# Kernel tuning notes

Measured on AMD Instinct MI355X. Metric: run time of the kernel, lower is better.

The kernel has to match this reference:

```python
import jax, jax.numpy as jnp
import numpy as np

N = 100000      # nodes
E = 3200000     # edges (avg degree 32)
F_IN = 16       # node_feature_size
R1, R2, R3 = 8, 16, 8   # gcn hidden sizes
N1 = 32                  # mlp hidden


def _lin(k, fan_in, shape):
    s = 1.0 / np.sqrt(fan_in)
    return jax.random.uniform(k, shape, minval=-s, maxval=s, dtype=jnp.float32)


def setup_inputs() -> dict:
    key = jax.random.key(0)
    ks = jax.random.split(key, 16)
    x = jax.random.normal(ks[0], (N, F_IN), dtype=jnp.float32)
    edge_index = jax.random.randint(ks[1], (2, E), 0, N, dtype=jnp.int64)
    return {
        "x": x,
        "edge_index": edge_index,
        # GraphConv k: out = mean_agg(x_j) @ W_rel + b + x @ W_root  (PyG GraphConv, lin_root bias=False)
        "W_rel1": _lin(ks[2], F_IN, (F_IN, R1)), "b1": _lin(ks[3], F_IN, (R1,)), "W_root1": _lin(ks[4], F_IN, (F_IN, R1)),
        "W_rel2": _lin(ks[5], R1, (R1, R2)),   "b2": _lin(ks[6], R1, (R2,)),   "W_root2": _lin(ks[7], R1, (R1, R2)),
        "W_rel3": _lin(ks[8], R2, (R2, R3)),   "b3": _lin(ks[9], R2, (R3,)),   "W_root3": _lin(ks[10], R2, (R2, R3)),
        "fc1_W": _lin(ks[11], R3, (R3, N1)), "fc1_b": _lin(ks[12], R3, (N1,)),
        "fc2_W": _lin(ks[13], N1, (N1, 1)),  "fc2_b": _lin(ks[14], N1, (1,)),
    }


def _graph_conv(x, src, dst, W_rel, b, W_root):
    # message: gather source features; aggregate: mean over incoming edges at dst
    n = x.shape[0]
    msg_sum = jax.ops.segment_sum(x[src], dst, num_segments=n)          # [N, F]
    cnt = jax.ops.segment_sum(jnp.ones(src.shape, x.dtype), dst, num_segments=n)
    mean = msg_sum / jnp.maximum(cnt, 1.0)[:, None]
    return mean @ W_rel + b + x @ W_root


def reference(x, edge_index, W_rel1, b1, W_root1, W_rel2, b2, W_root2,
              W_rel3, b3, W_root3, fc1_W, fc1_b, fc2_W, fc2_b):
    src, dst = edge_index[0], edge_index[1]
    h = jax.nn.sigmoid(_graph_conv(x, src, dst, W_rel1, b1, W_root1))
    h = jax.nn.sigmoid(_graph_conv(h, src, dst, W_rel2, b2, W_root2))
    h = jax.nn.sigmoid(_graph_conv(h, src, dst, W_rel3, b3, W_root3))
    h = jax.nn.sigmoid(h @ fc1_W + fc1_b)
    return h @ fc2_W + fc2_b   # [N, 1]
```

## Files before the change

### kernel.cpp

```cpp
#include <hip/hip_runtime.h>
#include <math.h>


#define CHUNK     16384
#define BW        128
#define MAXNB     800
#define MAXB_RAW  5376
#define MAXB_PAD  5760
#define REGION    5760

typedef _Float16 half8 __attribute__((ext_vector_type(8)));

static __device__ __forceinline__ float sigmoidf_(float x) {
    return 1.0f / (1.0f + expf(-x));
}

static __device__ __forceinline__ int scan256_excl(int v, int* s) {
    int tid = threadIdx.x;
    s[tid] = v;
    for (int off = 1; off < 256; off <<= 1) {
        __syncthreads();
        int t = (tid >= off) ? s[tid - off] : 0;
        __syncthreads();
        s[tid] += t;
    }
    __syncthreads();
    return s[tid] - v;
}

static __device__ __forceinline__ void gather_sum8(
    const half8* __restrict__ t, const int* __restrict__ csr,
    int rs, int from, int to, float* s) {
#pragma unroll
    for (int c = 0; c < 8; ++c) s[c] = 0.0f;
    int e = from;
    for (; e + 4 <= to; e += 4) {
        int4 ci = *(const int4*)(csr + rs + e);
        half8 v0 = t[ci.x]; half8 v1 = t[ci.y];
        half8 v2 = t[ci.z]; half8 v3 = t[ci.w];
#pragma unroll
        for (int c = 0; c < 8; ++c)
            s[c] += ((float)v0[c] + (float)v1[c]) + ((float)v2[c] + (float)v3[c]);
    }
    for (; e < to; ++e) {
        half8 v = t[csr[rs + e]];
#pragma unroll
        for (int c = 0; c < 8; ++c) s[c] += (float)v[c];
    }
}

static __device__ __forceinline__ void quad_gather_mean8(
    const half8* __restrict__ t, const int* __restrict__ csr,
    int rs, int d, int q, float* s) {
    int qs = ((d + 15) >> 4) << 2;
    int from = q * qs; if (from > d) from = d;
    int to = from + qs; if (to > d) to = d;
    gather_sum8(t, csr, rs, from, to, s);
#pragma unroll
    for (int c = 0; c < 8; ++c) s[c] += __shfl_xor(s[c], 1);
#pragma unroll
    for (int c = 0; c < 8; ++c) s[c] += __shfl_xor(s[c], 2);
    float inv = 1.0f / (float)(d > 0 ? d : 1);
#pragma unroll
    for (int c = 0; c < 8; ++c) s[c] *= inv;
}

__global__ __launch_bounds__(512)
void setup_scatter_kernel(const float* __restrict__ x, const float* __restrict__ Wrel,
                          const float* __restrict__ bias, const float* __restrict__ Wroot,
                          _Float16* __restrict__ t1, _Float16* __restrict__ z1,
                          const int* __restrict__ src, const int* __restrict__ dst,
                          int* __restrict__ gcur, unsigned* __restrict__ stage,
                          int N, int E, int NB, int nbT) {
    __shared__ float sWr[128], sWo[128], sb[8];
    __shared__ int s_hist[MAXNB];
    __shared__ int s_cur[MAXNB];
    int tid = threadIdx.x, blk = blockIdx.x;

    if (blk < nbT) {
        if (tid < 128) { sWr[tid] = Wrel[tid]; sWo[tid] = Wroot[tid]; }
        if (tid >= 128 && tid < 136) sb[tid - 128] = bias[tid - 128];
        __syncthreads();
        int node = blk * 512 + tid;
        if (node >= N) return;
        const float4* x4 = (const float4*)x;
        float xv[16];
#pragma unroll
        for (int k = 0; k < 4; ++k) {
            float4 v = x4[node * 4 + k];
            xv[4 * k] = v.x; xv[4 * k + 1] = v.y; xv[4 * k + 2] = v.z; xv[4 * k + 3] = v.w;
        }
        float ta[8], za[8];
#pragma unroll
        for (int j = 0; j < 8; ++j) { ta[j] = 0.0f; za[j] = sb[j]; }
#pragma unroll
        for (int f = 0; f < 16; ++f) {
            float xf = xv[f];
#pragma unroll
            for (int j = 0; j < 8; ++j) {
                ta[j] += xf * sWr[f * 8 + j];
                za[j] += xf * sWo[f * 8 + j];
            }
        }
        half8 th, zh;
#pragma unroll
        for (int j = 0; j < 8; ++j) { th[j] = (_Float16)ta[j]; zh[j] = (_Float16)za[j]; }
        ((half8*)t1)[node] = th;
        ((half8*)z1)[node] = zh;
    } else {
        int chunk = blk - nbT;
        int base = chunk * CHUNK;
        int cnt = E - base; if (cnt > CHUNK) cnt = CHUNK;
        for (int i = tid; i < NB; i += 512) s_hist[i] = 0;
        __syncthreads();
        if (cnt == CHUNK) {
            const int4* d4 = (const int4*)(dst + base);
#pragma unroll
            for (int k = 0; k < CHUNK / 2048; ++k) {
                int4 d = d4[k * 512 + tid];
                atomicAdd(&s_hist[d.x >> 7], 1);
                atomicAdd(&s_hist[d.y >> 7], 1);
                atomicAdd(&s_hist[d.z >> 7], 1);
                atomicAdd(&s_hist[d.w >> 7], 1);
            }
        } else {
            for (int i = tid; i < cnt; i += 512) atomicAdd(&s_hist[dst[base + i] >> 7], 1);
        }
        __syncthreads();
        for (int i = tid; i < NB; i += 512) {
            int hh = s_hist[i];
            s_cur[i] = i * REGION + atomicAdd(&gcur[i], hh);
        }
        __syncthreads();
        if (cnt == CHUNK) {
            const int4* d4 = (const int4*)(dst + base);
            const int4* s4 = (const int4*)(src + base);
#pragma unroll
            for (int k = 0; k < CHUNK / 2048; ++k) {
                int4 d = d4[k * 512 + tid];
                int4 s = s4[k * 512 + tid];
                int dd[4] = {d.x, d.y, d.z, d.w};
                int ss[4] = {s.x, s.y, s.z, s.w};
#pragma unroll
                for (int j = 0; j < 4; ++j) {
                    int pos = atomicAdd(&s_cur[dd[j] >> 7], 1);
                    stage[pos] = ((unsigned)(dd[j] & 127) << 17) | (unsigned)ss[j];
                }
            }
        } else {
            for (int i = tid; i < cnt; i += 512) {
                int d = dst[base + i], s = src[base + i];
                int pos = atomicAdd(&s_cur[d >> 7], 1);
                stage[pos] = ((unsigned)(d & 127) << 17) | (unsigned)s;
            }
        }
    }
}

__global__ __launch_bounds__(256)
void csr_agg1_kernel(const unsigned* __restrict__ stage, const int* __restrict__ gcur,
                     int* __restrict__ csr, int* __restrict__ deg,
                     int* __restrict__ rowstart,
                     const _Float16* __restrict__ t1, const _Float16* __restrict__ z1,
                     _Float16* __restrict__ h1, int N) {
    __shared__ unsigned __attribute__((aligned(16))) s_p[MAXB_RAW];
    __shared__ int __attribute__((aligned(16))) s_out[MAXB_PAD];
    __shared__ int h[BW], hs[BW], curb[BW];
    __shared__ int s_scan[256];
    int b = blockIdx.x, tid = threadIdx.x;
    int beg = b * REGION;
    int tot = gcur[b]; if (tot > MAXB_RAW) tot = MAXB_RAW;

    const uint4* st4 = (const uint4*)(stage + beg);
    int n4 = tot >> 2;
    for (int i = tid; i < n4; i += 256) ((uint4*)s_p)[i] = st4[i];
    for (int i = (n4 << 2) + tid; i < tot; i += 256) s_p[i] = stage[beg + i];
    if (tid < BW) h[tid] = 0;
    __syncthreads();

    for (int i = tid; i < tot; i += 256) atomicAdd(&h[s_p[i] >> 17], 1);
    __syncthreads();

    int v = (tid < BW) ? ((h[tid] + 3) & ~3) : 0;
    int excl = scan256_excl(v, s_scan);
    int ptot = s_scan[255];
    int dg = 0, myStart = 0;
    if (tid < BW) {
        dg = h[tid]; myStart = excl;
        hs[tid] = myStart; curb[tid] = myStart;
        int node = b * BW + tid;
        if (node < N) { deg[node] = dg; rowstart[node] = beg + myStart; }
    }
    __syncthreads();

    for (int i = tid; i < tot; i += 256) {
        unsigned p = s_p[i];
        int pos = atomicAdd(&curb[p >> 17], 1);
        s_out[pos] = (int)(p & 0x1FFFF);
    }
    __syncthreads();

    if (ptot > MAXB_PAD) ptot = MAXB_PAD;
    int p4 = ptot >> 2;
    int4* csr4 = (int4*)(csr + beg);
    for (int i = tid; i < p4; i += 256) csr4[i] = ((const int4*)s_out)[i];

    int nd = tid >> 1, half = tid & 1;
    int node = b * BW + nd;
    if (node < N) {
        int rs = hs[nd], d = h[nd];
        int d1 = ((d >> 1) + 3) & ~3; if (d1 > d) d1 = d;
        int from = half ? d1 : 0;
        int to   = half ? d  : d1;
        const half8* t = (const half8*)t1;
        float s[8];
#pragma unroll
        for (int c = 0; c < 8; ++c) s[c] = 0.0f;
        int e = from;
        for (; e + 4 <= to; e += 4) {
            int4 ci = *(const int4*)(s_out + rs + e);
            half8 v0 = t[ci.x]; half8 v1 = t[ci.y];
            half8 v2 = t[ci.z]; half8 v3 = t[ci.w];
#pragma unroll
            for (int c = 0; c < 8; ++c)
                s[c] += ((float)v0[c] + (float)v1[c]) + ((float)v2[c] + (float)v3[c]);
        }
        for (; e < to; ++e) {
            half8 vv = t[s_out[rs + e]];
#pragma unroll
            for (int c = 0; c < 8; ++c) s[c] += (float)vv[c];
        }
#pragma unroll
        for (int c = 0; c < 8; ++c) s[c] += __shfl_xor(s[c], 1);
        if (half == 0) {
            float inv = 1.0f / (float)(d > 0 ? d : 1);
            half8 z = ((const half8*)z1)[node];
            half8 o;
#pragma unroll
            for (int c = 0; c < 8; ++c) o[c] = (_Float16)sigmoidf_(s[c] * inv + (float)z[c]);
            ((half8*)h1)[node] = o;
        }
    }
}

__global__ __launch_bounds__(256)
void gcn2_fused_kernel(const _Float16* __restrict__ h1,
                       const int* __restrict__ rowstart, const int* __restrict__ deg,
                       const int* __restrict__ csr,
                       const float* __restrict__ W2r, const float* __restrict__ b2,
                       const float* __restrict__ W2o,
                       const float* __restrict__ W3r, const float* __restrict__ b3,
                       const float* __restrict__ W3o,
                       _Float16* __restrict__ t3, _Float16* __restrict__ z3, int n) {
    __shared__ float sW2r[128], sW2o[128], sW3r[128], sW3o[128], sb2[16], sb3[8];
    int tid = threadIdx.x;
    if (tid < 128) {
        sW2r[tid] = W2r[tid]; sW2o[tid] = W2o[tid];
        sW3r[tid] = W3r[tid]; sW3o[tid] = W3o[tid];
    }
    if (tid < 16) sb2[tid] = b2[tid];
    if (tid < 8) sb3[tid] = b3[tid];
    __syncthreads();
    int idx = blockIdx.x * 256 + tid;
    int node = idx >> 2, q = idx & 3;
    if (node >= n) return;

    float m[8];
    quad_gather_mean8((const half8*)h1, csr, rowstart[node], deg[node], q, m);
    half8 sf = ((const half8*)h1)[node];
    float x8[8];
#pragma unroll
    for (int c = 0; c < 8; ++c) x8[c] = (float)sf[c];

    float v16[16];
#pragma unroll
    for (int j = 0; j < 16; ++j) {
        float a = sb2[j];
#pragma unroll
        for (int f = 0; f < 8; ++f)
            a += m[f] * sW2r[f * 16 + j] + x8[f] * sW2o[f * 16 + j];
        v16[j] = sigmoidf_(a);
    }
    float ta[8], za[8];
#pragma unroll
    for (int j = 0; j < 8; ++j) { ta[j] = 0.0f; za[j] = sb3[j]; }
#pragma unroll
    for (int f = 0; f < 16; ++f) {
        float hv = v16[f];
#pragma unroll
        for (int j = 0; j < 8; ++j) {
            ta[j] += hv * sW3r[f * 8 + j];
            za[j] += hv * sW3o[f * 8 + j];
        }
    }
    if (q) return;
    half8 th, zh;
#pragma unroll
    for (int j = 0; j < 8; ++j) { th[j] = (_Float16)ta[j]; zh[j] = (_Float16)za[j]; }
    ((half8*)t3)[node] = th;
    ((half8*)z3)[node] = zh;
}

__global__ __launch_bounds__(256)
void agg3_mlp_kernel(const _Float16* __restrict__ t3, const _Float16* __restrict__ z3,
                     const int* __restrict__ rowstart, const int* __restrict__ deg,
                     const int* __restrict__ csr,
                     const float* __restrict__ fc1W, const float* __restrict__ fc1b,
                     const float* __restrict__ fc2W, const float* __restrict__ fc2b,
                     float* __restrict__ out, int n) {
    __shared__ float sW1[256], sb1[32], sW2[32];
    __shared__ float sb2_;
    int tid = threadIdx.x;
    if (tid < 256) sW1[tid] = fc1W[tid];
    if (tid < 32) { sb1[tid] = fc1b[tid]; sW2[tid] = fc2W[tid]; }
    if (tid == 0) sb2_ = fc2b[0];
    __syncthreads();
    int idx = blockIdx.x * 256 + tid;
    int node = idx >> 2, q = idx & 3;
    if (node >= n) return;

    float s[8];
    quad_gather_mean8((const half8*)t3, csr, rowstart[node], deg[node], q, s);
    half8 z = ((const half8*)z3)[node];
    float h[8];
#pragma unroll
    for (int c = 0; c < 8; ++c) h[c] = sigmoidf_(s[c] + (float)z[c]);

    float acc = sb2_;
#pragma unroll
    for (int j = 0; j < 32; ++j) {
        float a = sb1[j];
#pragma unroll
        for (int f = 0; f < 8; ++f) a += h[f] * sW1[f * 32 + j];
        acc += sW2[j] * sigmoidf_(a);
    }
    if (q == 0) out[node] = acc;
}

extern "C" void kernel_launch(void* const* d_in, const int* in_sizes, int n_in,
                              void* d_out, int out_size, void* d_ws, size_t ws_size,
                              hipStream_t stream) {
    const float* x      = (const float*)d_in[0];
    const int*   ei     = (const int*)d_in[1];
    const float* Wrel1  = (const float*)d_in[2];
    const float* b1     = (const float*)d_in[3];
    const float* Wroot1 = (const float*)d_in[4];
    const float* Wrel2  = (const float*)d_in[5];
    const float* b2     = (const float*)d_in[6];
    const float* Wroot2 = (const float*)d_in[7];
    const float* Wrel3  = (const float*)d_in[8];
    const float* b3     = (const float*)d_in[9];
    const float* Wroot3 = (const float*)d_in[10];
    const float* fc1W   = (const float*)d_in[11];
    const float* fc1b   = (const float*)d_in[12];
    const float* fc2W   = (const float*)d_in[13];
    const float* fc2b   = (const float*)d_in[14];
    float* out = (float*)d_out;

    const int N = in_sizes[0] / 16;
    const int E = in_sizes[1] / 2;
    const int* e_src = ei;
    const int* e_dst = ei + E;

    const int NB   = (N + BW - 1) / BW;
    const int NBLK = (E + CHUNK - 1) / CHUNK;
    const int nbT  = (N + 511) / 512;
    const int nbQ  = (4 * N + 255) / 256;

    char* ws = (char*)d_ws;
    size_t off = 0;
    auto alloc = [&](size_t bytes) { char* p = ws + off; off += (bytes + 15) & ~size_t(15); return p; };
    unsigned* stage = (unsigned*)alloc((size_t)NB * REGION * 4);
    int* csr        = (int*)alloc((size_t)NB * REGION * 4);
    int* gcur       = (int*)alloc((size_t)NB * 4);
    int* deg        = (int*)alloc((size_t)N * 4);
    int* rowstart   = (int*)alloc((size_t)N * 4);
    _Float16* t1    = (_Float16*)alloc((size_t)N * 8 * 2);
    _Float16* z1    = (_Float16*)alloc((size_t)N * 8 * 2);
    _Float16* h1    = (_Float16*)alloc((size_t)N * 8 * 2);
    _Float16* t3    = (_Float16*)alloc((size_t)N * 8 * 2);
    _Float16* z3    = (_Float16*)alloc((size_t)N * 8 * 2);

    hipMemsetAsync(gcur, 0, (size_t)NB * 4, stream);

    setup_scatter_kernel<<<nbT + NBLK, 512, 0, stream>>>(
        x, Wrel1, b1, Wroot1, t1, z1, e_src, e_dst, gcur, stage, N, E, NB, nbT);
    csr_agg1_kernel<<<NB, 256, 0, stream>>>(stage, gcur, csr, deg, rowstart,
                                            t1, z1, h1, N);
    gcn2_fused_kernel<<<nbQ, 256, 0, stream>>>(h1, rowstart, deg, csr,
                                               Wrel2, b2, Wroot2, Wrel3, b3, Wroot3, t3, z3, N);
    agg3_mlp_kernel<<<nbQ, 256, 0, stream>>>(t3, z3, rowstart, deg, csr,
                                             fc1W, fc1b, fc2W, fc2b, out, N);
}
```

Before: 223.5 us.

## Fuse CSR build and three aggregation layers into one persistent kernel with grid barriers

Merges the CSR-build/layer-1 kernel, the layer-2/3 kernel and the final aggregation+MLP kernel into a single kernel. Grid-wide atomic barriers separate the layers, and each block keeps its bucket's CSR in shared memory so it is never written to or re-read from global memory. Buckets grow to 256 nodes with 512-thread blocks, so NB blocks are about 391, and all of them must be co-resident for the spin barrier to avoid deadlock. The raw staged pairs are no longer copied into LDS; they are read twice from global memory instead. The change removes two launches and the global CSR traffic, at the cost of the barrier waits and a deadlock risk if the blocks are not all resident.

```diff
diff --git a/kernel.cpp b/kernel.cpp
--- a/kernel.cpp
+++ b/kernel.cpp
@@ -2,12 +2,12 @@
 #include <math.h>
 
 
-#define CHUNK     16384
-#define BW        128
-#define MAXNB     800
-#define MAXB_RAW  5376
-#define MAXB_PAD  5760
-#define REGION    5760
+#define CHUNK    32768
+#define BW       256
+#define NBMAX    400
+#define MAXB_RAW 9216
+#define MAXB_PAD 9984
+#define REGION   9472
 
 typedef _Float16 half8 __attribute__((ext_vector_type(8)));
 
@@ -15,54 +15,15 @@
     return 1.0f / (1.0f + expf(-x));
 }
 
-static __device__ __forceinline__ int scan256_excl(int v, int* s) {
-    int tid = threadIdx.x;
-    s[tid] = v;
-    for (int off = 1; off < 256; off <<= 1) {
-        __syncthreads();
-        int t = (tid >= off) ? s[tid - off] : 0;
-        __syncthreads();
-        s[tid] += t;
-    }
-    __syncthreads();
-    return s[tid] - v;
-}
-
-static __device__ __forceinline__ void gather_sum8(
-    const half8* __restrict__ t, const int* __restrict__ csr,
-    int rs, int from, int to, float* s) {
-#pragma unroll
-    for (int c = 0; c < 8; ++c) s[c] = 0.0f;
-    int e = from;
-    for (; e + 4 <= to; e += 4) {
-        int4 ci = *(const int4*)(csr + rs + e);
-        half8 v0 = t[ci.x]; half8 v1 = t[ci.y];
-        half8 v2 = t[ci.z]; half8 v3 = t[ci.w];
-#pragma unroll
-        for (int c = 0; c < 8; ++c)
-            s[c] += ((float)v0[c] + (float)v1[c]) + ((float)v2[c] + (float)v3[c]);
-    }
-    for (; e < to; ++e) {
-        half8 v = t[csr[rs + e]];
-#pragma unroll
-        for (int c = 0; c < 8; ++c) s[c] += (float)v[c];
-    }
-}
-
-static __device__ __forceinline__ void quad_gather_mean8(
-    const half8* __restrict__ t, const int* __restrict__ csr,
-    int rs, int d, int q, float* s) {
-    int qs = ((d + 15) >> 4) << 2;
-    int from = q * qs; if (from > d) from = d;
-    int to = from + qs; if (to > d) to = d;
-    gather_sum8(t, csr, rs, from, to, s);
-#pragma unroll
-    for (int c = 0; c < 8; ++c) s[c] += __shfl_xor(s[c], 1);
-#pragma unroll
-    for (int c = 0; c < 8; ++c) s[c] += __shfl_xor(s[c], 2);
-    float inv = 1.0f / (float)(d > 0 ? d : 1);
-#pragma unroll
-    for (int c = 0; c < 8; ++c) s[c] *= inv;
+static __device__ __forceinline__ void gbar(int* bar, int target) {
+    __syncthreads();
+    if (threadIdx.x == 0) {
+        __threadfence();
+        __hip_atomic_fetch_add(bar, 1, __ATOMIC_ACQ_REL, __HIP_MEMORY_SCOPE_AGENT);
+        while (__hip_atomic_load(bar, __ATOMIC_ACQUIRE, __HIP_MEMORY_SCOPE_AGENT) < target)
+            __builtin_amdgcn_s_sleep(32);
+    }
+    __syncthreads();
 }
 
 __global__ __launch_bounds__(512)
@@ -73,8 +34,8 @@
                           int* __restrict__ gcur, unsigned* __restrict__ stage,
                           int N, int E, int NB, int nbT) {
     __shared__ float sWr[128], sWo[128], sb[8];
-    __shared__ int s_hist[MAXNB];
-    __shared__ int s_cur[MAXNB];
+    __shared__ int s_hist[NBMAX];
+    __shared__ int s_cur[NBMAX];
     int tid = threadIdx.x, blk = blockIdx.x;
 
     if (blk < nbT) {
@@ -118,13 +79,13 @@
 #pragma unroll
             for (int k = 0; k < CHUNK / 2048; ++k) {
                 int4 d = d4[k * 512 + tid];
-                atomicAdd(&s_hist[d.x >> 7], 1);
-                atomicAdd(&s_hist[d.y >> 7], 1);
-                atomicAdd(&s_hist[d.z >> 7], 1);
-                atomicAdd(&s_hist[d.w >> 7], 1);
+                atomicAdd(&s_hist[d.x >> 8], 1);
+                atomicAdd(&s_hist[d.y >> 8], 1);
+                atomicAdd(&s_hist[d.z >> 8], 1);
+                atomicAdd(&s_hist[d.w >> 8], 1);
             }
         } else {
-            for (int i = tid; i < cnt; i += 512) atomicAdd(&s_hist[dst[base + i] >> 7], 1);
+            for (int i = tid; i < cnt; i += 512) atomicAdd(&s_hist[dst[base + i] >> 8], 1);
         }
         __syncthreads();
         for (int i = tid; i < NB; i += 512) {
@@ -143,75 +104,102 @@
                 int ss[4] = {s.x, s.y, s.z, s.w};
 #pragma unroll
                 for (int j = 0; j < 4; ++j) {
-                    int pos = atomicAdd(&s_cur[dd[j] >> 7], 1);
-                    stage[pos] = ((unsigned)(dd[j] & 127) << 17) | (unsigned)ss[j];
+                    int pos = atomicAdd(&s_cur[dd[j] >> 8], 1);
+                    stage[pos] = ((unsigned)(dd[j] & 255) << 17) | (unsigned)ss[j];
                 }
             }
         } else {
             for (int i = tid; i < cnt; i += 512) {
                 int d = dst[base + i], s = src[base + i];
-                int pos = atomicAdd(&s_cur[d >> 7], 1);
-                stage[pos] = ((unsigned)(d & 127) << 17) | (unsigned)s;
-            }
-        }
-    }
-}
-
-__global__ __launch_bounds__(256)
-void csr_agg1_kernel(const unsigned* __restrict__ stage, const int* __restrict__ gcur,
-                     int* __restrict__ csr, int* __restrict__ deg,
-                     int* __restrict__ rowstart,
-                     const _Float16* __restrict__ t1, const _Float16* __restrict__ z1,
-                     _Float16* __restrict__ h1, int N) {
-    __shared__ unsigned __attribute__((aligned(16))) s_p[MAXB_RAW];
+                int pos = atomicAdd(&s_cur[d >> 8], 1);
+                stage[pos] = ((unsigned)(d & 255) << 17) | (unsigned)s;
+            }
+        }
+    }
+}
+
+__global__ __launch_bounds__(512, 4)
+void mega_kernel(const unsigned* __restrict__ stage, const int* __restrict__ gcur,
+                 int* __restrict__ bar,
+                 const _Float16* __restrict__ t1, const _Float16* __restrict__ z1,
+                 _Float16* __restrict__ h1, _Float16* __restrict__ t3,
+                 _Float16* __restrict__ z3,
+                 const float* __restrict__ W2r, const float* __restrict__ b2,
+                 const float* __restrict__ W2o,
+                 const float* __restrict__ W3r, const float* __restrict__ b3,
+                 const float* __restrict__ W3o,
+                 const float* __restrict__ fc1W, const float* __restrict__ fc1b,
+                 const float* __restrict__ fc2W, const float* __restrict__ fc2b,
+                 float* __restrict__ out, int N, int NB) {
     __shared__ int __attribute__((aligned(16))) s_out[MAXB_PAD];
     __shared__ int h[BW], hs[BW], curb[BW];
-    __shared__ int s_scan[256];
+    __shared__ int s_scan[512];
+    __shared__ float sW2r[128], sW2o[128], sW3r[128], sW3o[128], sb2[16], sb3[8];
+    __shared__ float sW1[256], sb1[32], sW2m[32], sb2s[1];
+
     int b = blockIdx.x, tid = threadIdx.x;
     int beg = b * REGION;
     int tot = gcur[b]; if (tot > MAXB_RAW) tot = MAXB_RAW;
 
+    if (tid < 128) { sW2r[tid] = W2r[tid]; sW2o[tid] = W2o[tid];
+                     sW3r[tid] = W3r[tid]; sW3o[tid] = W3o[tid]; }
+    if (tid < 256) sW1[tid] = fc1W[tid];
+    if (tid < 32) { sb1[tid] = fc1b[tid]; sW2m[tid] = fc2W[tid]; }
+    if (tid < 16) sb2[tid] = b2[tid];
+    if (tid < 8)  sb3[tid] = b3[tid];
+    if (tid == 0) sb2s[0] = fc2b[0];
+    if (tid < BW) h[tid] = 0;
+    __syncthreads();
+
     const uint4* st4 = (const uint4*)(stage + beg);
     int n4 = tot >> 2;
-    for (int i = tid; i < n4; i += 256) ((uint4*)s_p)[i] = st4[i];
-    for (int i = (n4 << 2) + tid; i < tot; i += 256) s_p[i] = stage[beg + i];
-    if (tid < BW) h[tid] = 0;
-    __syncthreads();
-
-    for (int i = tid; i < tot; i += 256) atomicAdd(&h[s_p[i] >> 17], 1);
+    for (int i = tid; i < n4; i += 512) {
+        uint4 p = st4[i];
+        atomicAdd(&h[p.x >> 17], 1); atomicAdd(&h[p.y >> 17], 1);
+        atomicAdd(&h[p.z >> 17], 1); atomicAdd(&h[p.w >> 17], 1);
+    }
+    for (int i = (n4 << 2) + tid; i < tot; i += 512) atomicAdd(&h[stage[beg + i] >> 17], 1);
     __syncthreads();
 
     int v = (tid < BW) ? ((h[tid] + 3) & ~3) : 0;
-    int excl = scan256_excl(v, s_scan);
-    int ptot = s_scan[255];
-    int dg = 0, myStart = 0;
-    if (tid < BW) {
-        dg = h[tid]; myStart = excl;
-        hs[tid] = myStart; curb[tid] = myStart;
-        int node = b * BW + tid;
-        if (node < N) { deg[node] = dg; rowstart[node] = beg + myStart; }
-    }
-    __syncthreads();
-
-    for (int i = tid; i < tot; i += 256) {
-        unsigned p = s_p[i];
+    s_scan[tid] = v;
+    for (int off = 1; off < 512; off <<= 1) {
+        __syncthreads();
+        int t = (tid >= off) ? s_scan[tid - off] : 0;
+        __syncthreads();
+        s_scan[tid] += t;
+    }
+    __syncthreads();
+    if (tid < BW) { int myS = s_scan[tid] - v; hs[tid] = myS; curb[tid] = myS; }
+    __syncthreads();
+
+    for (int i = tid; i < n4; i += 512) {
+        uint4 p = st4[i];
+        int pos;
+        pos = atomicAdd(&curb[p.x >> 17], 1); s_out[pos] = (int)(p.x & 0x1FFFF);
+        pos = atomicAdd(&curb[p.y >> 17], 1); s_out[pos] = (int)(p.y & 0x1FFFF);
+        pos = atomicAdd(&curb[p.z >> 17], 1); s_out[pos] = (int)(p.z & 0x1FFFF);
+        pos = atomicAdd(&curb[p.w >> 17], 1); s_out[pos] = (int)(p.w & 0x1FFFF);
+    }
+    for (int i = (n4 << 2) + tid; i < tot; i += 512) {
+        unsigned p = stage[beg + i];
         int pos = atomicAdd(&curb[p >> 17], 1);
         s_out[pos] = (int)(p & 0x1FFFF);
     }
     __syncthreads();
 
-    if (ptot > MAXB_PAD) ptot = MAXB_PAD;
-    int p4 = ptot >> 2;
-    int4* csr4 = (int4*)(csr + beg);
-    for (int i = tid; i < p4; i += 256) csr4[i] = ((const int4*)s_out)[i];
-
     int nd = tid >> 1, half = tid & 1;
     int node = b * BW + nd;
+    int rs = 0, d = 0, from = 0, to = 0;
     if (node < N) {
-        int rs = hs[nd], d = h[nd];
+        rs = hs[nd]; d = h[nd];
         int d1 = ((d >> 1) + 3) & ~3; if (d1 > d) d1 = d;
-        int from = half ? d1 : 0;
-        int to   = half ? d  : d1;
+        from = half ? d1 : 0;
+        to   = half ? d  : d1;
+    }
+    float inv = 1.0f / (float)(d > 0 ? d : 1);
+
+    if (node < N) {
         const half8* t = (const half8*)t1;
         float s[8];
 #pragma unroll
@@ -219,8 +207,7 @@
         int e = from;
         for (; e + 4 <= to; e += 4) {
             int4 ci = *(const int4*)(s_out + rs + e);
-            half8 v0 = t[ci.x]; half8 v1 = t[ci.y];
-            half8 v2 = t[ci.z]; half8 v3 = t[ci.w];
+            half8 v0 = t[ci.x], v1 = t[ci.y], v2 = t[ci.z], v3 = t[ci.w];
 #pragma unroll
             for (int c = 0; c < 8; ++c)
                 s[c] += ((float)v0[c] + (float)v1[c]) + ((float)v2[c] + (float)v3[c]);
@@ -233,7 +220,6 @@
 #pragma unroll
         for (int c = 0; c < 8; ++c) s[c] += __shfl_xor(s[c], 1);
         if (half == 0) {
-            float inv = 1.0f / (float)(d > 0 ? d : 1);
             half8 z = ((const half8*)z1)[node];
             half8 o;
 #pragma unroll
@@ -241,100 +227,100 @@
             ((half8*)h1)[node] = o;
         }
     }
-}
-
-__global__ __launch_bounds__(256)
-void gcn2_fused_kernel(const _Float16* __restrict__ h1,
-                       const int* __restrict__ rowstart, const int* __restrict__ deg,
-                       const int* __restrict__ csr,
-                       const float* __restrict__ W2r, const float* __restrict__ b2,
-                       const float* __restrict__ W2o,
-                       const float* __restrict__ W3r, const float* __restrict__ b3,
-                       const float* __restrict__ W3o,
-                       _Float16* __restrict__ t3, _Float16* __restrict__ z3, int n) {
-    __shared__ float sW2r[128], sW2o[128], sW3r[128], sW3o[128], sb2[16], sb3[8];
-    int tid = threadIdx.x;
-    if (tid < 128) {
-        sW2r[tid] = W2r[tid]; sW2o[tid] = W2o[tid];
-        sW3r[tid] = W3r[tid]; sW3o[tid] = W3o[tid];
-    }
-    if (tid < 16) sb2[tid] = b2[tid];
-    if (tid < 8) sb3[tid] = b3[tid];
-    __syncthreads();
-    int idx = blockIdx.x * 256 + tid;
-    int node = idx >> 2, q = idx & 3;
-    if (node >= n) return;
-
-    float m[8];
-    quad_gather_mean8((const half8*)h1, csr, rowstart[node], deg[node], q, m);
-    half8 sf = ((const half8*)h1)[node];
-    float x8[8];
-#pragma unroll
-    for (int c = 0; c < 8; ++c) x8[c] = (float)sf[c];
-
-    float v16[16];
-#pragma unroll
-    for (int j = 0; j < 16; ++j) {
-        float a = sb2[j];
-#pragma unroll
-        for (int f = 0; f < 8; ++f)
-            a += m[f] * sW2r[f * 16 + j] + x8[f] * sW2o[f * 16 + j];
-        v16[j] = sigmoidf_(a);
-    }
-    float ta[8], za[8];
-#pragma unroll
-    for (int j = 0; j < 8; ++j) { ta[j] = 0.0f; za[j] = sb3[j]; }
-#pragma unroll
-    for (int f = 0; f < 16; ++f) {
-        float hv = v16[f];
-#pragma unroll
-        for (int j = 0; j < 8; ++j) {
-            ta[j] += hv * sW3r[f * 8 + j];
-            za[j] += hv * sW3o[f * 8 + j];
-        }
-    }
-    if (q) return;
-    half8 th, zh;
-#pragma unroll
-    for (int j = 0; j < 8; ++j) { th[j] = (_Float16)ta[j]; zh[j] = (_Float16)za[j]; }
-    ((half8*)t3)[node] = th;
-    ((half8*)z3)[node] = zh;
-}
-
-__global__ __launch_bounds__(256)
-void agg3_mlp_kernel(const _Float16* __restrict__ t3, const _Float16* __restrict__ z3,
-                     const int* __restrict__ rowstart, const int* __restrict__ deg,
-                     const int* __restrict__ csr,
-                     const float* __restrict__ fc1W, const float* __restrict__ fc1b,
-                     const float* __restrict__ fc2W, const float* __restrict__ fc2b,
-                     float* __restrict__ out, int n) {
-    __shared__ float sW1[256], sb1[32], sW2[32];
-    __shared__ float sb2_;
-    int tid = threadIdx.x;
-    if (tid < 256) sW1[tid] = fc1W[tid];
-    if (tid < 32) { sb1[tid] = fc1b[tid]; sW2[tid] = fc2W[tid]; }
-    if (tid == 0) sb2_ = fc2b[0];
-    __syncthreads();
-    int idx = blockIdx.x * 256 + tid;
-    int node = idx >> 2, q = idx & 3;
-    if (node >= n) return;
-
-    float s[8];
-    quad_gather_mean8((const half8*)t3, csr, rowstart[node], deg[node], q, s);
-    half8 z = ((const half8*)z3)[node];
-    float h[8];
-#pragma unroll
-    for (int c = 0; c < 8; ++c) h[c] = sigmoidf_(s[c] + (float)z[c]);
-
-    float acc = sb2_;
-#pragma unroll
-    for (int j = 0; j < 32; ++j) {
-        float a = sb1[j];
-#pragma unroll
-        for (int f = 0; f < 8; ++f) a += h[f] * sW1[f * 32 + j];
-        acc += sW2[j] * sigmoidf_(a);
-    }
-    if (q == 0) out[node] = acc;
+    gbar(bar, NB);
+
+    if (node < N) {
+        const half8* t = (const half8*)h1;
+        float s[8];
+#pragma unroll
+        for (int c = 0; c < 8; ++c) s[c] = 0.0f;
+        int e = from;
+        for (; e + 4 <= to; e += 4) {
+            int4 ci = *(const int4*)(s_out + rs + e);
+            half8 v0 = t[ci.x], v1 = t[ci.y], v2 = t[ci.z], v3 = t[ci.w];
+#pragma unroll
+            for (int c = 0; c < 8; ++c)
+                s[c] += ((float)v0[c] + (float)v1[c]) + ((float)v2[c] + (float)v3[c]);
+        }
+        for (; e < to; ++e) {
+            half8 vv = t[s_out[rs + e]];
+#pragma unroll
+            for (int c = 0; c < 8; ++c) s[c] += (float)vv[c];
+        }
+#pragma unroll
+        for (int c = 0; c < 8; ++c) s[c] += __shfl_xor(s[c], 1);
+        float m[8];
+#pragma unroll
+        for (int c = 0; c < 8; ++c) m[c] = s[c] * inv;
+        half8 sf = ((const half8*)h1)[node];
+        float x8[8];
+#pragma unroll
+        for (int c = 0; c < 8; ++c) x8[c] = (float)sf[c];
+        float v16[16];
+#pragma unroll
+        for (int j = 0; j < 16; ++j) {
+            float a = sb2[j];
+#pragma unroll
+            for (int f = 0; f < 8; ++f)
+                a += m[f] * sW2r[f * 16 + j] + x8[f] * sW2o[f * 16 + j];
+            v16[j] = sigmoidf_(a);
+        }
+        float ta[8], za[8];
+#pragma unroll
+        for (int j = 0; j < 8; ++j) { ta[j] = 0.0f; za[j] = sb3[j]; }
+#pragma unroll
+        for (int f = 0; f < 16; ++f) {
+            float hv = v16[f];
+#pragma unroll
+            for (int j = 0; j < 8; ++j) {
+                ta[j] += hv * sW3r[f * 8 + j];
+                za[j] += hv * sW3o[f * 8 + j];
+            }
+        }
+        if (half == 0) {
+            half8 th, zh;
+#pragma unroll
+            for (int j = 0; j < 8; ++j) { th[j] = (_Float16)ta[j]; zh[j] = (_Float16)za[j]; }
+            ((half8*)t3)[node] = th;
+            ((half8*)z3)[node] = zh;
+        }
+    }
+    gbar(bar, 2 * NB);
+
+    if (node < N) {
+        const half8* t = (const half8*)t3;
+        float s[8];
+#pragma unroll
+        for (int c = 0; c < 8; ++c) s[c] = 0.0f;
+        int e = from;
+        for (; e + 4 <= to; e += 4) {
+            int4 ci = *(const int4*)(s_out + rs + e);
+            half8 v0 = t[ci.x], v1 = t[ci.y], v2 = t[ci.z], v3 = t[ci.w];
+#pragma unroll
+            for (int c = 0; c < 8; ++c)
+                s[c] += ((float)v0[c] + (float)v1[c]) + ((float)v2[c] + (float)v3[c]);
+        }
+        for (; e < to; ++e) {
+            half8 vv = t[s_out[rs + e]];
+#pragma unroll
+            for (int c = 0; c < 8; ++c) s[c] += (float)vv[c];
+        }
+#pragma unroll
+        for (int c = 0; c < 8; ++c) s[c] += __shfl_xor(s[c], 1);
+        half8 z = ((const half8*)z3)[node];
+        float hv8[8];
+#pragma unroll
+        for (int c = 0; c < 8; ++c) hv8[c] = sigmoidf_(s[c] * inv + (float)z[c]);
+        float acc = sb2s[0];
+#pragma unroll
+        for (int j = 0; j < 32; ++j) {
+            float a = sb1[j];
+#pragma unroll
+            for (int f = 0; f < 8; ++f) a += hv8[f] * sW1[f * 32 + j];
+            acc += sW2m[j] * sigmoidf_(a);
+        }
+        if (half == 0) out[node] = acc;
+    }
 }
 
 extern "C" void kernel_launch(void* const* d_in, const int* in_sizes, int n_in,
@@ -365,30 +351,26 @@
     const int NB   = (N + BW - 1) / BW;
     const int NBLK = (E + CHUNK - 1) / CHUNK;
     const int nbT  = (N + 511) / 512;
-    const int nbQ  = (4 * N + 255) / 256;
 
     char* ws = (char*)d_ws;
     size_t off = 0;
     auto alloc = [&](size_t bytes) { char* p = ws + off; off += (bytes + 15) & ~size_t(15); return p; };
     unsigned* stage = (unsigned*)alloc((size_t)NB * REGION * 4);
-    int* csr        = (int*)alloc((size_t)NB * REGION * 4);
-    int* gcur       = (int*)alloc((size_t)NB * 4);
-    int* deg        = (int*)alloc((size_t)N * 4);
-    int* rowstart   = (int*)alloc((size_t)N * 4);
+    int* gcur       = (int*)alloc(((size_t)NB + 8) * 4);
+    int* bar        = gcur + NB;
     _Float16* t1    = (_Float16*)alloc((size_t)N * 8 * 2);
     _Float16* z1    = (_Float16*)alloc((size_t)N * 8 * 2);
     _Float16* h1    = (_Float16*)alloc((size_t)N * 8 * 2);
     _Float16* t3    = (_Float16*)alloc((size_t)N * 8 * 2);
     _Float16* z3    = (_Float16*)alloc((size_t)N * 8 * 2);
 
-    hipMemsetAsync(gcur, 0, (size_t)NB * 4, stream);
+    hipMemsetAsync(gcur, 0, ((size_t)NB + 8) * 4, stream);
 
     setup_scatter_kernel<<<nbT + NBLK, 512, 0, stream>>>(
         x, Wrel1, b1, Wroot1, t1, z1, e_src, e_dst, gcur, stage, N, E, NB, nbT);
-    csr_agg1_kernel<<<NB, 256, 0, stream>>>(stage, gcur, csr, deg, rowstart,
-                                            t1, z1, h1, N);
-    gcn2_fused_kernel<<<nbQ, 256, 0, stream>>>(h1, rowstart, deg, csr,
-                                               Wrel2, b2, Wroot2, Wrel3, b3, Wroot3, t3, z3, N);
-    agg3_mlp_kernel<<<nbQ, 256, 0, stream>>>(t3, z3, rowstart, deg, csr,
-                                             fc1W, fc1b, fc2W, fc2b, out, N);
-}
+
+    mega_kernel<<<NB, 512, 0, stream>>>(
+        stage, gcur, bar, t1, z1, h1, t3, z3,
+        Wrel2, b2, Wroot2, Wrel3, b3, Wroot3,
+        fc1W, fc1b, fc2W, fc2b, out, N, NB);
+}
```

Measured after the change: 337.3 us. +50.9%, slower.

## Widen per-node gather parallelism and double scatter chunk size

Applied to the files above, without the earlier changes.

Doubles the edge chunk size in the scatter stage. The CSR/aggregation-1 kernel moves to 512 threads, using four lanes per node instead of two. Layer-2 and final aggregation kernels use eight lanes per node instead of four, and non-leader lanes return early after the reduction so the dense tail math runs once per node. The aim is more memory-level parallelism in the latency-bound gathers and less redundant per-lane compute, at the cost of an extra shuffle stage, a longer block scan and fewer scatter blocks.

```diff
diff --git a/kernel.cpp b/kernel.cpp
--- a/kernel.cpp
+++ b/kernel.cpp
@@ -2,7 +2,7 @@
 #include <math.h>
 
 
-#define CHUNK     16384
+#define CHUNK     32768
 #define BW        128
 #define MAXNB     800
 #define MAXB_RAW  5376
@@ -13,19 +13,6 @@
 
 static __device__ __forceinline__ float sigmoidf_(float x) {
     return 1.0f / (1.0f + expf(-x));
-}
-
-static __device__ __forceinline__ int scan256_excl(int v, int* s) {
-    int tid = threadIdx.x;
-    s[tid] = v;
-    for (int off = 1; off < 256; off <<= 1) {
-        __syncthreads();
-        int t = (tid >= off) ? s[tid - off] : 0;
-        __syncthreads();
-        s[tid] += t;
-    }
-    __syncthreads();
-    return s[tid] - v;
 }
 
 static __device__ __forceinline__ void gather_sum8(
@@ -49,17 +36,19 @@
     }
 }
 
-static __device__ __forceinline__ void quad_gather_mean8(
+static __device__ __forceinline__ void oct_gather_mean8(
     const half8* __restrict__ t, const int* __restrict__ csr,
-    int rs, int d, int q, float* s) {
-    int qs = ((d + 15) >> 4) << 2;
-    int from = q * qs; if (from > d) from = d;
+    int rs, int d, int oc, float* s) {
+    int qs = ((d + 31) >> 5) << 2;
+    int from = oc * qs; if (from > d) from = d;
     int to = from + qs; if (to > d) to = d;
     gather_sum8(t, csr, rs, from, to, s);
 #pragma unroll
     for (int c = 0; c < 8; ++c) s[c] += __shfl_xor(s[c], 1);
 #pragma unroll
     for (int c = 0; c < 8; ++c) s[c] += __shfl_xor(s[c], 2);
+#pragma unroll
+    for (int c = 0; c < 8; ++c) s[c] += __shfl_xor(s[c], 4);
     float inv = 1.0f / (float)(d > 0 ? d : 1);
 #pragma unroll
     for (int c = 0; c < 8; ++c) s[c] *= inv;
@@ -157,7 +146,7 @@
     }
 }
 
-__global__ __launch_bounds__(256)
+__global__ __launch_bounds__(512)
 void csr_agg1_kernel(const unsigned* __restrict__ stage, const int* __restrict__ gcur,
                      int* __restrict__ csr, int* __restrict__ deg,
                      int* __restrict__ rowstart,
@@ -166,34 +155,40 @@
     __shared__ unsigned __attribute__((aligned(16))) s_p[MAXB_RAW];
     __shared__ int __attribute__((aligned(16))) s_out[MAXB_PAD];
     __shared__ int h[BW], hs[BW], curb[BW];
-    __shared__ int s_scan[256];
+    __shared__ int s_scan[512];
     int b = blockIdx.x, tid = threadIdx.x;
     int beg = b * REGION;
     int tot = gcur[b]; if (tot > MAXB_RAW) tot = MAXB_RAW;
 
     const uint4* st4 = (const uint4*)(stage + beg);
     int n4 = tot >> 2;
-    for (int i = tid; i < n4; i += 256) ((uint4*)s_p)[i] = st4[i];
-    for (int i = (n4 << 2) + tid; i < tot; i += 256) s_p[i] = stage[beg + i];
+    for (int i = tid; i < n4; i += 512) ((uint4*)s_p)[i] = st4[i];
+    for (int i = (n4 << 2) + tid; i < tot; i += 512) s_p[i] = stage[beg + i];
     if (tid < BW) h[tid] = 0;
     __syncthreads();
 
-    for (int i = tid; i < tot; i += 256) atomicAdd(&h[s_p[i] >> 17], 1);
+    for (int i = tid; i < tot; i += 512) atomicAdd(&h[s_p[i] >> 17], 1);
     __syncthreads();
 
     int v = (tid < BW) ? ((h[tid] + 3) & ~3) : 0;
-    int excl = scan256_excl(v, s_scan);
-    int ptot = s_scan[255];
-    int dg = 0, myStart = 0;
+    s_scan[tid] = v;
+    for (int off = 1; off < 512; off <<= 1) {
+        __syncthreads();
+        int t = (tid >= off) ? s_scan[tid - off] : 0;
+        __syncthreads();
+        s_scan[tid] += t;
+    }
+    __syncthreads();
+    int ptot = s_scan[511];
     if (tid < BW) {
-        dg = h[tid]; myStart = excl;
-        hs[tid] = myStart; curb[tid] = myStart;
+        int myS = s_scan[tid] - v;
+        hs[tid] = myS; curb[tid] = myS;
         int node = b * BW + tid;
-        if (node < N) { deg[node] = dg; rowstart[node] = beg + myStart; }
-    }
-    __syncthreads();
-
-    for (int i = tid; i < tot; i += 256) {
+        if (node < N) { deg[node] = h[tid]; rowstart[node] = beg + myS; }
+    }
+    __syncthreads();
+
+    for (int i = tid; i < tot; i += 512) {
         unsigned p = s_p[i];
         int pos = atomicAdd(&curb[p >> 17], 1);
         s_out[pos] = (int)(p & 0x1FFFF);
@@ -203,15 +198,15 @@
     if (ptot > MAXB_PAD) ptot = MAXB_PAD;
     int p4 = ptot >> 2;
     int4* csr4 = (int4*)(csr + beg);
-    for (int i = tid; i < p4; i += 256) csr4[i] = ((const int4*)s_out)[i];
-
-    int nd = tid >> 1, half = tid & 1;
+    for (int i = tid; i < p4; i += 512) csr4[i] = ((const int4*)s_out)[i];
+
+    int nd = tid >> 2, q = tid & 3;
     int node = b * BW + nd;
     if (node < N) {
         int rs = hs[nd], d = h[nd];
-        int d1 = ((d >> 1) + 3) & ~3; if (d1 > d) d1 = d;
-        int from = half ? d1 : 0;
-        int to   = half ? d  : d1;
+        int qs = ((d + 15) >> 4) << 2;
+        int from = q * qs; if (from > d) from = d;
+        int to = from + qs; if (to > d) to = d;
         const half8* t = (const half8*)t1;
         float s[8];
 #pragma unroll
@@ -232,7 +227,9 @@
         }
 #pragma unroll
         for (int c = 0; c < 8; ++c) s[c] += __shfl_xor(s[c], 1);
-        if (half == 0) {
+#pragma unroll
+        for (int c = 0; c < 8; ++c) s[c] += __shfl_xor(s[c], 2);
+        if (q == 0) {
             float inv = 1.0f / (float)(d > 0 ? d : 1);
             half8 z = ((const half8*)z1)[node];
             half8 o;
@@ -262,11 +259,11 @@
     if (tid < 8) sb3[tid] = b3[tid];
     __syncthreads();
     int idx = blockIdx.x * 256 + tid;
-    int node = idx >> 2, q = idx & 3;
+    int node = idx >> 3, oc = idx & 7;
     if (node >= n) return;
 
     float m[8];
-    quad_gather_mean8((const half8*)h1, csr, rowstart[node], deg[node], q, m);
+    oct_gather_mean8((const half8*)h1, csr, rowstart[node], deg[node], oc, m);
     half8 sf = ((const half8*)h1)[node];
     float x8[8];
 #pragma unroll
@@ -281,6 +278,7 @@
             a += m[f] * sW2r[f * 16 + j] + x8[f] * sW2o[f * 16 + j];
         v16[j] = sigmoidf_(a);
     }
+    if (oc) return;
     float ta[8], za[8];
 #pragma unroll
     for (int j = 0; j < 8; ++j) { ta[j] = 0.0f; za[j] = sb3[j]; }
@@ -293,7 +291,6 @@
             za[j] += hv * sW3o[f * 8 + j];
         }
     }
-    if (q) return;
     half8 th, zh;
 #pragma unroll
     for (int j = 0; j < 8; ++j) { th[j] = (_Float16)ta[j]; zh[j] = (_Float16)za[j]; }
@@ -316,11 +313,12 @@
     if (tid == 0) sb2_ = fc2b[0];
     __syncthreads();
     int idx = blockIdx.x * 256 + tid;
-    int node = idx >> 2, q = idx & 3;
+    int node = idx >> 3, oc = idx & 7;
     if (node >= n) return;
 
     float s[8];
-    quad_gather_mean8((const half8*)t3, csr, rowstart[node], deg[node], q, s);
+    oct_gather_mean8((const half8*)t3, csr, rowstart[node], deg[node], oc, s);
+    if (oc) return;
     half8 z = ((const half8*)z3)[node];
     float h[8];
 #pragma unroll
@@ -334,7 +332,7 @@
         for (int f = 0; f < 8; ++f) a += h[f] * sW1[f * 32 + j];
         acc += sW2[j] * sigmoidf_(a);
     }
-    if (q == 0) out[node] = acc;
+    out[node] = acc;
 }
 
 extern "C" void kernel_launch(void* const* d_in, const int* in_sizes, int n_in,
@@ -365,7 +363,7 @@
     const int NB   = (N + BW - 1) / BW;
     const int NBLK = (E + CHUNK - 1) / CHUNK;
     const int nbT  = (N + 511) / 512;
-    const int nbQ  = (4 * N + 255) / 256;
+    const int nbO  = (8 * N + 255) / 256;
 
     char* ws = (char*)d_ws;
     size_t off = 0;
@@ -385,10 +383,10 @@
 
     setup_scatter_kernel<<<nbT + NBLK, 512, 0, stream>>>(
         x, Wrel1, b1, Wroot1, t1, z1, e_src, e_dst, gcur, stage, N, E, NB, nbT);
-    csr_agg1_kernel<<<NB, 256, 0, stream>>>(stage, gcur, csr, deg, rowstart,
+    csr_agg1_kernel<<<NB, 512, 0, stream>>>(stage, gcur, csr, deg, rowstart,
                                             t1, z1, h1, N);
-    gcn2_fused_kernel<<<nbQ, 256, 0, stream>>>(h1, rowstart, deg, csr,
+    gcn2_fused_kernel<<<nbO, 256, 0, stream>>>(h1, rowstart, deg, csr,
                                                Wrel2, b2, Wroot2, Wrel3, b3, Wroot3, t3, z3, N);
-    agg3_mlp_kernel<<<nbQ, 256, 0, stream>>>(t3, z3, rowstart, deg, csr,
+    agg3_mlp_kernel<<<nbO, 256, 0, stream>>>(t3, z3, rowstart, deg, csr,
                                              fc1W, fc1b, fc2W, fc2b, out, N);
 }
```

After: 256.8 us. 1.15x slower.
